# Performance work log

Hardware: AMD Instinct MI355X
Metric: run time of the kernel (lower is better)

## Reference

```python
import jax, jax.numpy as jnp
import numpy as np

EPS = 1e-12
HEADS = 16
DIM_KEYS = 16
DIM_VALUES = 64


def l2norm(t):
    # matches F.normalize(t, p=2, dim=-1) with eps=1e-12
    n = jnp.linalg.norm(t, axis=-1, keepdims=True)
    return t / jnp.maximum(n, EPS)


def tanh_norm(t):
    n = jnp.linalg.norm(t, axis=-1, keepdims=True)
    return jnp.tanh(n) * (t / jnp.maximum(n, EPS))


def split_heads(x, h):
    # [b, n, h*d] -> [b, h, n, d]
    b, n, hd = x.shape
    return x.reshape(b, n, h, hd // h).transpose(0, 2, 1, 3)


def setup_inputs() -> dict:
    key = jax.random.key(0)
    k1, k2, k3, k4 = jax.random.split(key, 4)
    b, n, dim = 4, 2048, 1024
    dim_inner = (DIM_KEYS + DIM_VALUES) * HEADS  # 1280
    tokens = jax.random.normal(k1, (b, n, dim), dtype=jnp.float32)
    Wqg = jax.random.normal(k2, (dim, dim_inner), dtype=jnp.float32) * (dim ** -0.5)
    Wkv = jax.random.normal(k3, (dim, dim_inner), dtype=jnp.float32) * (dim ** -0.5)
    Wout = jax.random.normal(k4, (DIM_VALUES * HEADS, dim), dtype=jnp.float32) * ((DIM_VALUES * HEADS) ** -0.5)
    return {"tokens": tokens, "Wqg": Wqg, "Wkv": Wkv, "Wout": Wout}


def reference(tokens, Wqg, Wkv, Wout):
    # self-attention variant: context = tokens, mask = None
    qg = split_heads(tokens @ Wqg, HEADS)   # [b, h, n, dk+dv]
    kv = split_heads(tokens @ Wkv, HEADS)
    queries, gates = qg[..., :DIM_KEYS], qg[..., DIM_KEYS:]
    keys, values = kv[..., :DIM_KEYS], kv[..., DIM_KEYS:]
    queries, keys, values = l2norm(queries), l2norm(keys), l2norm(values)
    sim = jnp.einsum('bhid,bhjd->bhij', queries, keys)
    attn = jnp.square(jax.nn.relu(sim))
    aggr = jnp.einsum('bhij,bhjd->bhid', attn, values)
    out = tanh_norm(aggr) * jnp.tanh(jax.nn.silu(gates))
    b, h, n, d = out.shape
    out = out.transpose(0, 2, 1, 3).reshape(b, n, h * d)  # merge heads
    return out @ Wout
```

## Files before the change

### kernel.cpp

```cpp
#include <hip/hip_runtime.h>
#include <cstdint>
#include <cstddef>

typedef __attribute__((ext_vector_type(8))) short short8;
typedef __attribute__((ext_vector_type(8))) unsigned short ushort8;
typedef __attribute__((ext_vector_type(4))) float f32x4;
typedef __attribute__((ext_vector_type(8))) _Float16 half8;
typedef __attribute__((ext_vector_type(2))) __fp16 fp16x2;

#define DEV static __device__ __forceinline__

DEV unsigned short f2bf(float x) {
  union { float f; unsigned u; } v; v.f = x;
  unsigned r = v.u + 0x7fffu + ((v.u >> 16) & 1u);
  return (unsigned short)(r >> 16);
}
DEV float bf2f(unsigned short u) {
  union { unsigned u; float f; } v; v.u = ((unsigned)u) << 16;
  return v.f;
}
DEV unsigned pack2bf(float lo, float hi) {
  union { float f; unsigned u; } a, b; a.f = lo; b.f = hi;
  return __builtin_amdgcn_perm(b.u + 0x8000u, a.u + 0x8000u, 0x07060302u);
}
DEV f32x4 mfma16(short8 a, short8 b, f32x4 c) {
  return __builtin_amdgcn_mfma_f32_16x16x32_bf16(a, b, c, 0, 0, 0);
}
DEV f32x4 mfma16h(half8 a, half8 b, f32x4 c) {
  return __builtin_amdgcn_mfma_f32_16x16x32_f16(a, b, c, 0, 0, 0);
}

typedef __attribute__((address_space(1))) unsigned int g_u32;
typedef __attribute__((address_space(3))) unsigned int l_u32;
DEV void glds16(const unsigned short* g, unsigned short* l) {
  __builtin_amdgcn_global_load_lds((g_u32*)g, (l_u32*)l, 16, 0, 0);
}

constexpr int Bc = 4, Nc = 2048, Dc = 1024, Hc = 16, DKc = 16, DVc = 64, DIc = 1280;
constexpr int Mc = Bc * Nc;

__global__ __launch_bounds__(256) void convert_x(const float* __restrict__ X,
                                                 unsigned short* __restrict__ Xb, int total8) {
  int i = blockIdx.x * 256 + threadIdx.x;
  if (i >= total8) return;
  const float4* p = (const float4*)(X + (size_t)i * 8);
  float4 a = p[0], b = p[1];
  ushort8 o;
  o[0] = f2bf(a.x); o[1] = f2bf(a.y); o[2] = f2bf(a.z); o[3] = f2bf(a.w);
  o[4] = f2bf(b.x); o[5] = f2bf(b.y); o[6] = f2bf(b.z); o[7] = f2bf(b.w);
  *(ushort8*)(Xb + (size_t)i * 8) = o;
}

__global__ __launch_bounds__(256) void transpose_convert(const float* __restrict__ W,
                                                         unsigned short* __restrict__ WT,
                                                         int K, int N) {
  __shared__ unsigned short t[64][72];
  int k0 = blockIdx.x * 64, n0 = blockIdx.y * 64;
  int tid = threadIdx.x;
#pragma unroll
  for (int it = 0; it < 16; ++it) {
    int f = it * 256 + tid;
    int r = f >> 6, c = f & 63;
    t[c][r] = f2bf(W[(size_t)(k0 + r) * N + n0 + c]);
  }
  __syncthreads();
#pragma unroll
  for (int it = 0; it < 16; ++it) {
    int f = it * 256 + tid;
    int r = f >> 6, c = f & 63;
    WT[(size_t)(n0 + r) * K + k0 + c] = t[r][c];
  }
}

__global__ __launch_bounds__(256) void gemm_proj(const unsigned short* __restrict__ A,
                                                 const unsigned short* __restrict__ BT,
                                                 unsigned short* __restrict__ QG,
                                                 unsigned short* __restrict__ KV,
                                                 int Kq) {
  __shared__ unsigned short As[128 * 64];
  __shared__ unsigned short Bs[128 * 64];
  int row0 = blockIdx.x * 128, col0 = blockIdx.y * 128;
  int tid = threadIdx.x, lane = tid & 63, wave = tid >> 6;
  int wm = wave >> 1, wn = wave & 1;
  int ql = lane >> 4, l16 = lane & 15;
  int r8 = lane >> 3, cbl = (lane & 7) ^ r8;

  unsigned short* dst = (col0 >= DIc) ? KV : QG;
  int c0l = (col0 >= DIc) ? col0 - DIc : col0;

  const unsigned short* gA = A + (size_t)(row0 + wave * 32 + r8) * Kq + cbl * 8;
  const unsigned short* gB = BT + (size_t)(col0 + wave * 32 + r8) * Kq + cbl * 8;

  f32x4 acc[4][4];
#pragma unroll
  for (int i = 0; i < 4; i++)
#pragma unroll
    for (int j = 0; j < 4; j++) acc[i][j] = (f32x4){0.f, 0.f, 0.f, 0.f};

  for (int k0 = 0; k0 < Kq; k0 += 64) {
    __syncthreads();
#pragma unroll
    for (int i = 0; i < 4; ++i) {
      glds16(gA + (size_t)(i * 8) * Kq + k0, &As[(wave * 32 + i * 8) * 64]);
      glds16(gB + (size_t)(i * 8) * Kq + k0, &Bs[(wave * 32 + i * 8) * 64]);
    }
    __syncthreads();
#pragma unroll
    for (int kk = 0; kk < 64; kk += 32) {
      short8 af[4], bfr[4];
#pragma unroll
      for (int t = 0; t < 4; t++) {
        int row = wm * 64 + t * 16 + l16;
        int cb = (kk >> 3) + ql;
        af[t] = *(const short8*)&As[row * 64 + ((cb ^ (row & 7)) << 3)];
      }
#pragma unroll
      for (int t = 0; t < 4; t++) {
        int row = wn * 64 + t * 16 + l16;
        int cb = (kk >> 3) + ql;
        bfr[t] = *(const short8*)&Bs[row * 64 + ((cb ^ (row & 7)) << 3)];
      }
#pragma unroll
      for (int i = 0; i < 4; i++)
#pragma unroll
        for (int j = 0; j < 4; j++) acc[i][j] = mfma16(af[i], bfr[j], acc[i][j]);
    }
  }
#pragma unroll
  for (int i = 0; i < 4; i++)
#pragma unroll
    for (int j = 0; j < 4; j++)
#pragma unroll
      for (int r = 0; r < 4; r++) {
        int rr = row0 + wm * 64 + i * 16 + ql * 4 + r;
        int cc = c0l + wn * 64 + j * 16 + l16;
        dst[(size_t)rr * DIc + cc] = f2bf(acc[i][j][r]);
      }
}

__global__ __launch_bounds__(256) void gemm_glds(const unsigned short* __restrict__ A,
                                                 const unsigned short* __restrict__ BT,
                                                 float* __restrict__ Cout,
                                                 int Mq, int Nq, int Kq) {
  __shared__ unsigned short As[128 * 64];
  __shared__ unsigned short Bs[128 * 64];
  int row0 = blockIdx.x * 128, col0 = blockIdx.y * 128;
  int tid = threadIdx.x, lane = tid & 63, wave = tid >> 6;
  int wm = wave >> 1, wn = wave & 1;
  int ql = lane >> 4, l16 = lane & 15;
  int r8 = lane >> 3, cbl = (lane & 7) ^ r8;

  const unsigned short* gA = A + (size_t)(row0 + wave * 32 + r8) * Kq + cbl * 8;
  const unsigned short* gB = BT + (size_t)(col0 + wave * 32 + r8) * Kq + cbl * 8;

  f32x4 acc[4][4];
#pragma unroll
  for (int i = 0; i < 4; i++)
#pragma unroll
    for (int j = 0; j < 4; j++) acc[i][j] = (f32x4){0.f, 0.f, 0.f, 0.f};

  for (int k0 = 0; k0 < Kq; k0 += 64) {
    __syncthreads();
#pragma unroll
    for (int i = 0; i < 4; ++i) {
      glds16(gA + (size_t)(i * 8) * Kq + k0, &As[(wave * 32 + i * 8) * 64]);
      glds16(gB + (size_t)(i * 8) * Kq + k0, &Bs[(wave * 32 + i * 8) * 64]);
    }
    __syncthreads();
#pragma unroll
    for (int kk = 0; kk < 64; kk += 32) {
      short8 af[4], bfr[4];
#pragma unroll
      for (int t = 0; t < 4; t++) {
        int row = wm * 64 + t * 16 + l16;
        int cb = (kk >> 3) + ql;
        af[t] = *(const short8*)&As[row * 64 + ((cb ^ (row & 7)) << 3)];
      }
#pragma unroll
      for (int t = 0; t < 4; t++) {
        int row = wn * 64 + t * 16 + l16;
        int cb = (kk >> 3) + ql;
        bfr[t] = *(const short8*)&Bs[row * 64 + ((cb ^ (row & 7)) << 3)];
      }
#pragma unroll
      for (int i = 0; i < 4; i++)
#pragma unroll
        for (int j = 0; j < 4; j++) acc[i][j] = mfma16(af[i], bfr[j], acc[i][j]);
    }
  }
#pragma unroll
  for (int i = 0; i < 4; i++)
#pragma unroll
    for (int j = 0; j < 4; j++)
#pragma unroll
      for (int r = 0; r < 4; r++) {
        int rr = row0 + wm * 64 + i * 16 + ql * 4 + r;
        int cc = col0 + wn * 64 + j * 16 + l16;
        Cout[(size_t)rr * Nq + cc] = acc[i][j][r];
      }
}

__global__ __launch_bounds__(256) void norm_kernel(const unsigned short* __restrict__ QG,
                                                   const unsigned short* __restrict__ KV,
                                                   unsigned short* __restrict__ Qn,
                                                   unsigned short* __restrict__ Kn,
                                                   unsigned short* __restrict__ Vtg)
{
  int g = blockIdx.x * 256 + threadIdx.x;
  int n = g & (Nc - 1), bh = g >> 11;
  int h = bh & 15, b = bh >> 4;
  size_t src = ((size_t)(b * Nc + n)) * DIc + h * 80;
  const ushort8 zeros = {0, 0, 0, 0, 0, 0, 0, 0};

  {
    ushort8 u0 = *(const ushort8*)&QG[src];
    ushort8 u1 = *(const ushort8*)&QG[src + 8];
    float q[16], ss = 0.f;
#pragma unroll
    for (int i = 0; i < 8; i++) { q[i] = bf2f(u0[i]); q[8 + i] = bf2f(u1[i]); }
#pragma unroll
    for (int i = 0; i < 16; i++) ss += q[i] * q[i];
    float sc = 1.f / fmaxf(sqrtf(ss), 1e-12f);
    half8 o0, o1;
#pragma unroll
    for (int i = 0; i < 8; i++) { o0[i] = (_Float16)(q[i] * sc); o1[i] = (_Float16)(q[8 + i] * sc); }
    size_t dst = ((size_t)bh * Nc + n) * 32;
    *(half8*)&Qn[dst] = o0;
    *(half8*)&Qn[dst + 8] = o1;
    *(ushort8*)&Qn[dst + 16] = zeros;
    *(ushort8*)&Qn[dst + 24] = zeros;
  }
  {
    ushort8 u0 = *(const ushort8*)&KV[src];
    ushort8 u1 = *(const ushort8*)&KV[src + 8];
    float q[16], ss = 0.f;
#pragma unroll
    for (int i = 0; i < 8; i++) { q[i] = bf2f(u0[i]); q[8 + i] = bf2f(u1[i]); }
#pragma unroll
    for (int i = 0; i < 16; i++) ss += q[i] * q[i];
    float sc = 1.f / fmaxf(sqrtf(ss), 1e-12f);
    half8 o0, o1;
#pragma unroll
    for (int i = 0; i < 8; i++) { o0[i] = (_Float16)(q[i] * sc); o1[i] = (_Float16)(q[8 + i] * sc); }
    size_t dst = ((size_t)bh * Nc + n) * 32;
    *(half8*)&Kn[dst] = o0;
    *(half8*)&Kn[dst + 8] = o1;
    *(ushort8*)&Kn[dst + 16] = zeros;
    *(ushort8*)&Kn[dst + 24] = zeros;
  }
  {
    ushort8 u[8];
#pragma unroll
    for (int i = 0; i < 8; i++) u[i] = *(const ushort8*)&KV[src + 16 + i * 8];
    float ss = 0.f;
#pragma unroll
    for (int i = 0; i < 8; i++)
#pragma unroll
      for (int j = 0; j < 8; j++) { float x = bf2f(u[i][j]); ss += x * x; }
    float sc = 1.f / fmaxf(sqrtf(ss), 1e-12f);
#pragma unroll
    for (int i = 0; i < 8; i++)
#pragma unroll
      for (int j = 0; j < 8; j++) {
        int d = i * 8 + j;
        union { _Float16 h; unsigned short us; } cv;
        cv.h = (_Float16)(bf2f(u[i][j]) * sc);
        Vtg[((size_t)bh * DVc + d) * Nc + n] = cv.us;
      }
  }
}

__global__ __launch_bounds__(256, 4) void attn_kernel(const unsigned short* __restrict__ Qn,
                                                      const unsigned short* __restrict__ Kn,
                                                      const unsigned short* __restrict__ Vtg,
                                                      const unsigned short* __restrict__ QG,
                                                      unsigned short* __restrict__ outpre) {
  __shared__ unsigned short shm[2 * 64 * 128];

  int gid = blockIdx.x;
  int xcd = gid & 7, slot = gid >> 3;
  int bh = xcd * 8 + (slot & 7);
  int q0 = (slot >> 3) * 128;
  int b = bh >> 4, h = bh & 15;
  int tid = threadIdx.x, lane = tid & 63, wave = tid >> 6;
  int ql = lane >> 4, l16 = lane & 15;
  int qw0 = q0 + wave * 32;

  half8 qf[2];
#pragma unroll
  for (int qt = 0; qt < 2; ++qt)
    qf[qt] = *(const half8*)&Qn[((size_t)bh * Nc + qw0 + qt * 16 + l16) * 32 + ql * 8];

  const unsigned short* krow = Kn + ((size_t)bh * Nc) * 32;
  const unsigned short* vbase = Vtg + ((size_t)bh * DVc) * Nc;

  int lr = lane >> 4, m16 = lane & 15;

  f32x4 acc[4][2];
#pragma unroll
  for (int dt = 0; dt < 4; dt++) { acc[dt][0] = (f32x4){0.f,0.f,0.f,0.f}; acc[dt][1] = (f32x4){0.f,0.f,0.f,0.f}; }

#pragma unroll
  for (int i = 0; i < 4; ++i) {
    int r0 = i * 16 + wave * 4;
    int d = r0 + lr;
    glds16(vbase + (size_t)d * Nc + 0 + ((m16 ^ (d & 7)) << 3), &shm[r0 * 128]);
  }

  for (int kt = 0; kt < Nc / 128; ++kt) {
    int k0 = kt * 128;
    unsigned short* vtb = &shm[(kt & 1) * 8192];
    __syncthreads();

    half8 kf[8];
#pragma unroll
    for (int kh = 0; kh < 8; ++kh)
      kf[kh] = *(const half8*)&krow[(size_t)(k0 + kh * 16 + l16) * 32 + ql * 8];

    if (kt < Nc / 128 - 1) {
      unsigned short* nb = &shm[((kt + 1) & 1) * 8192];
      int kn0 = k0 + 128;
#pragma unroll
      for (int i = 0; i < 4; ++i) {
        int r0 = i * 16 + wave * 4;
        int d = r0 + lr;
        glds16(vbase + (size_t)d * Nc + kn0 + ((m16 ^ (d & 7)) << 3), &nb[r0 * 128]);
      }
    }

#pragma unroll
    for (int p = 0; p < 4; ++p) {
      f32x4 c0[2], c1[2];
#pragma unroll
      for (int qt = 0; qt < 2; ++qt) {
        c0[qt] = mfma16h(kf[2 * p], qf[qt], (f32x4){0.f, 0.f, 0.f, 0.f});
        c1[qt] = mfma16h(kf[2 * p + 1], qf[qt], (f32x4){0.f, 0.f, 0.f, 0.f});
      }
      half8 pf[2];
#pragma unroll
      for (int qt = 0; qt < 2; ++qt) {
        union { half8 h; fp16x2 p2[4]; } w;
        fp16x2 t0 = __builtin_amdgcn_cvt_pkrtz(c0[qt][0], c0[qt][1]);
        fp16x2 t1 = __builtin_amdgcn_cvt_pkrtz(c0[qt][2], c0[qt][3]);
        fp16x2 t2 = __builtin_amdgcn_cvt_pkrtz(c1[qt][0], c1[qt][1]);
        fp16x2 t3 = __builtin_amdgcn_cvt_pkrtz(c1[qt][2], c1[qt][3]);
        const fp16x2 hz = {(__fp16)0, (__fp16)0};
        t0 = __builtin_elementwise_max(t0, hz); w.p2[0] = t0 * t0;
        t1 = __builtin_elementwise_max(t1, hz); w.p2[1] = t1 * t1;
        t2 = __builtin_elementwise_max(t2, hz); w.p2[2] = t2 * t2;
        t3 = __builtin_elementwise_max(t3, hz); w.p2[3] = t3 * t3;
        pf[qt] = w.h;
      }
      int tsw = (l16 & 7) << 1;
      int s1 = ((p * 8 + ql) ^ tsw) << 2;
      int s2 = ((p * 8 + 4 + ql) ^ tsw) << 2;
#pragma unroll
      for (int dt = 0; dt < 4; ++dt) {
        const unsigned short* vrow = vtb + (dt * 16 + l16) * 128;
        union { half8 s; uint4 u; } vf;
        uint2 va = *(const uint2*)&vrow[s1];
        uint2 vb2 = *(const uint2*)&vrow[s2];
        vf.u.x = va.x; vf.u.y = va.y; vf.u.z = vb2.x; vf.u.w = vb2.y;
#pragma unroll
        for (int qt = 0; qt < 2; ++qt) acc[dt][qt] = mfma16h(vf.s, pf[qt], acc[dt][qt]);
      }
    }
  }

  __syncthreads();
  unsigned short(*of)[68] = (unsigned short(*)[68])shm;

#pragma unroll
  for (int qt = 0; qt < 2; ++qt) {
    float ss = 0.f;
#pragma unroll
    for (int dt = 0; dt < 4; ++dt)
#pragma unroll
      for (int r = 0; r < 4; ++r) { float v = acc[dt][qt][r]; ss += v * v; }
    ss += __shfl_xor(ss, 16, 64);
    ss += __shfl_xor(ss, 32, 64);
    float nrm = sqrtf(ss);
    float sc = tanhf(nrm) / fmaxf(nrm, 1e-12f);
    int q = qw0 + qt * 16 + l16;
    size_t gbase = ((size_t)(b * Nc + q)) * DIc + h * 80 + DKc;
#pragma unroll
    for (int dt = 0; dt < 4; ++dt) {
      uint2 gu = *(const uint2*)&QG[gbase + dt * 16 + ql * 4];
      float o[4];
#pragma unroll
      for (int r = 0; r < 4; ++r) {
        unsigned short gb = (r < 2) ? (unsigned short)(gu.x >> (16 * r))
                                    : (unsigned short)(gu.y >> (16 * (r - 2)));
        float x = bf2f(gb);
        float s = x / (1.f + __expf(-x));
        float e2 = __expf(2.f * s);
        float g = 1.f - 2.f / (e2 + 1.f);
        o[r] = acc[dt][qt][r] * sc * g;
      }
      uint2 w;
      w.x = pack2bf(o[0], o[1]);
      w.y = pack2bf(o[2], o[3]);
      *(uint2*)&of[wave * 32 + qt * 16 + l16][dt * 16 + ql * 4] = w;
    }
  }
  __syncthreads();
  {
    int row = tid >> 1, cb = (tid & 1) * 32;
    size_t obase = ((size_t)(b * Nc + q0 + row)) * (Hc * DVc) + h * DVc + cb;
#pragma unroll
    for (int i = 0; i < 4; ++i)
      *(ushort8*)&outpre[obase + i * 8] = *(const ushort8*)&of[row][cb + i * 8];
  }
}

extern "C" void kernel_launch(void* const* d_in, const int* in_sizes, int n_in,
                              void* d_out, int out_size, void* d_ws, size_t ws_size,
                              hipStream_t stream) {
  const float* X = (const float*)d_in[0];
  const float* Wqg = (const float*)d_in[1];
  const float* Wkv = (const float*)d_in[2];
  const float* Wout = (const float*)d_in[3];
  float* out = (float*)d_out;
  (void)in_sizes; (void)n_in; (void)out_size; (void)ws_size;

  char* ws = (char*)d_ws;
  size_t off = 0;
  auto alloc = [&](size_t bytes) {
    void* p = ws + off;
    off += (bytes + 255) & ~(size_t)255;
    return p;
  };
  unsigned short* Xbf   = (unsigned short*)alloc((size_t)Mc * Dc * 2);
  unsigned short* WqgT  = (unsigned short*)alloc((size_t)DIc * Dc * 2);
  unsigned short* WkvT  = (unsigned short*)alloc((size_t)DIc * Dc * 2);
  unsigned short* WoutT = (unsigned short*)alloc((size_t)Dc * Dc * 2);
  unsigned short* QG    = (unsigned short*)alloc((size_t)Mc * DIc * 2);
  unsigned short* KV    = (unsigned short*)alloc((size_t)Mc * DIc * 2);
  unsigned short* Qn    = (unsigned short*)alloc((size_t)Bc * Hc * Nc * 32 * 2);
  unsigned short* Kn    = (unsigned short*)alloc((size_t)Bc * Hc * Nc * 32 * 2);
  unsigned short* Vtg   = (unsigned short*)alloc((size_t)Bc * Hc * Nc * DVc * 2);
  unsigned short* outpre = Xbf;

  convert_x<<<(Mc * Dc / 8) / 256, 256, 0, stream>>>(X, Xbf, Mc * Dc / 8);
  transpose_convert<<<dim3(Dc / 64, DIc / 64), 256, 0, stream>>>(Wqg, WqgT, Dc, DIc);
  transpose_convert<<<dim3(Dc / 64, DIc / 64), 256, 0, stream>>>(Wkv, WkvT, Dc, DIc);
  transpose_convert<<<dim3(Dc / 64, Dc / 64), 256, 0, stream>>>(Wout, WoutT, Dc, Dc);
  gemm_proj<<<dim3(Mc / 128, 2 * DIc / 128), 256, 0, stream>>>(Xbf, WqgT, QG, KV, Dc);
  norm_kernel<<<(Mc * Hc) / 256, 256, 0, stream>>>(QG, KV, Qn, Kn, Vtg);
  attn_kernel<<<1024, 256, 0, stream>>>(Qn, Kn, Vtg, QG, outpre);
  gemm_glds<<<dim3(Mc / 128, Dc / 128), 256, 0, stream>>>(outpre, WoutT, out, Mc, Dc, Dc);
}
```

Baseline: 262.3 us.

## Drop zero-padded Q/K, use 16x16x16 MFMA, register-staged V prefetch pipeline

Q and K are now stored as 16 fp16 values per row instead of being zero-padded to 32, which halves their memory footprint and the norm kernel's writes. The QK^T step uses the 16x16x16 f16 MFMA so no work is spent on the zero padding. V tiles are prefetched into registers and written to LDS with a new swizzle after compute, replacing the async global_load_lds path. The K-tile loop is unrolled by two with ping-pong K fragment registers, and s_setprio is raised around the PV MFMAs. The register staging raises register pressure, and the changed swizzle has to stay consistent between the LDS writes and reads.

```diff
diff --git a/kernel.cpp b/kernel.cpp
--- a/kernel.cpp
+++ b/kernel.cpp
@@ -6,6 +6,7 @@
 typedef __attribute__((ext_vector_type(8))) unsigned short ushort8;
 typedef __attribute__((ext_vector_type(4))) float f32x4;
 typedef __attribute__((ext_vector_type(8))) _Float16 half8;
+typedef __attribute__((ext_vector_type(4))) _Float16 half4;
 typedef __attribute__((ext_vector_type(2))) __fp16 fp16x2;
 
 #define DEV static __device__ __forceinline__
@@ -28,6 +29,9 @@
 }
 DEV f32x4 mfma16h(half8 a, half8 b, f32x4 c) {
   return __builtin_amdgcn_mfma_f32_16x16x32_f16(a, b, c, 0, 0, 0);
+}
+DEV f32x4 mfma16k(half4 a, half4 b, f32x4 c) {
+  return __builtin_amdgcn_mfma_f32_16x16x16f16(a, b, c, 0, 0, 0);
 }
 
 typedef __attribute__((address_space(1))) unsigned int g_u32;
@@ -210,7 +214,6 @@
   int n = g & (Nc - 1), bh = g >> 11;
   int h = bh & 15, b = bh >> 4;
   size_t src = ((size_t)(b * Nc + n)) * DIc + h * 80;
-  const ushort8 zeros = {0, 0, 0, 0, 0, 0, 0, 0};
 
   {
     ushort8 u0 = *(const ushort8*)&QG[src];
@@ -224,11 +227,9 @@
     half8 o0, o1;
 #pragma unroll
     for (int i = 0; i < 8; i++) { o0[i] = (_Float16)(q[i] * sc); o1[i] = (_Float16)(q[8 + i] * sc); }
-    size_t dst = ((size_t)bh * Nc + n) * 32;
+    size_t dst = ((size_t)bh * Nc + n) * 16;
     *(half8*)&Qn[dst] = o0;
     *(half8*)&Qn[dst + 8] = o1;
-    *(ushort8*)&Qn[dst + 16] = zeros;
-    *(ushort8*)&Qn[dst + 24] = zeros;
   }
   {
     ushort8 u0 = *(const ushort8*)&KV[src];
@@ -242,11 +243,9 @@
     half8 o0, o1;
 #pragma unroll
     for (int i = 0; i < 8; i++) { o0[i] = (_Float16)(q[i] * sc); o1[i] = (_Float16)(q[8 + i] * sc); }
-    size_t dst = ((size_t)bh * Nc + n) * 32;
+    size_t dst = ((size_t)bh * Nc + n) * 16;
     *(half8*)&Kn[dst] = o0;
     *(half8*)&Kn[dst + 8] = o1;
-    *(ushort8*)&Kn[dst + 16] = zeros;
-    *(ushort8*)&Kn[dst + 24] = zeros;
   }
   {
     ushort8 u[8];
@@ -286,86 +285,110 @@
   int ql = lane >> 4, l16 = lane & 15;
   int qw0 = q0 + wave * 32;
 
-  half8 qf[2];
+  half4 qf[2];
 #pragma unroll
   for (int qt = 0; qt < 2; ++qt)
-    qf[qt] = *(const half8*)&Qn[((size_t)bh * Nc + qw0 + qt * 16 + l16) * 32 + ql * 8];
-
-  const unsigned short* krow = Kn + ((size_t)bh * Nc) * 32;
+    qf[qt] = *(const half4*)&Qn[((size_t)bh * Nc + qw0 + qt * 16 + l16) * 16 + ql * 4];
+
+  const unsigned short* krow = Kn + (size_t)bh * Nc * 16;
   const unsigned short* vbase = Vtg + ((size_t)bh * DVc) * Nc;
 
-  int lr = lane >> 4, m16 = lane & 15;
+  int lq = lane >> 4, m16 = lane & 15;
+  unsigned swp = (unsigned)(lq & 1);
 
   f32x4 acc[4][2];
 #pragma unroll
   for (int dt = 0; dt < 4; dt++) { acc[dt][0] = (f32x4){0.f,0.f,0.f,0.f}; acc[dt][1] = (f32x4){0.f,0.f,0.f,0.f}; }
 
-#pragma unroll
-  for (int i = 0; i < 4; ++i) {
-    int r0 = i * 16 + wave * 4;
-    int d = r0 + lr;
-    glds16(vbase + (size_t)d * Nc + 0 + ((m16 ^ (d & 7)) << 3), &shm[r0 * 128]);
-  }
-
-  for (int kt = 0; kt < Nc / 128; ++kt) {
-    int k0 = kt * 128;
-    unsigned short* vtb = &shm[(kt & 1) * 8192];
-    __syncthreads();
-
-    half8 kf[8];
-#pragma unroll
-    for (int kh = 0; kh < 8; ++kh)
-      kf[kh] = *(const half8*)&krow[(size_t)(k0 + kh * 16 + l16) * 32 + ql * 8];
-
-    if (kt < Nc / 128 - 1) {
-      unsigned short* nb = &shm[((kt + 1) & 1) * 8192];
-      int kn0 = k0 + 128;
-#pragma unroll
-      for (int i = 0; i < 4; ++i) {
-        int r0 = i * 16 + wave * 4;
-        int d = r0 + lr;
-        glds16(vbase + (size_t)d * Nc + kn0 + ((m16 ^ (d & 7)) << 3), &nb[r0 * 128]);
-      }
-    }
-
-#pragma unroll
-    for (int p = 0; p < 4; ++p) {
-      f32x4 c0[2], c1[2];
-#pragma unroll
-      for (int qt = 0; qt < 2; ++qt) {
-        c0[qt] = mfma16h(kf[2 * p], qf[qt], (f32x4){0.f, 0.f, 0.f, 0.f});
-        c1[qt] = mfma16h(kf[2 * p + 1], qf[qt], (f32x4){0.f, 0.f, 0.f, 0.f});
-      }
-      half8 pf[2];
-#pragma unroll
-      for (int qt = 0; qt < 2; ++qt) {
-        union { half8 h; fp16x2 p2[4]; } w;
-        fp16x2 t0 = __builtin_amdgcn_cvt_pkrtz(c0[qt][0], c0[qt][1]);
-        fp16x2 t1 = __builtin_amdgcn_cvt_pkrtz(c0[qt][2], c0[qt][3]);
-        fp16x2 t2 = __builtin_amdgcn_cvt_pkrtz(c1[qt][0], c1[qt][1]);
-        fp16x2 t3 = __builtin_amdgcn_cvt_pkrtz(c1[qt][2], c1[qt][3]);
-        const fp16x2 hz = {(__fp16)0, (__fp16)0};
-        t0 = __builtin_elementwise_max(t0, hz); w.p2[0] = t0 * t0;
-        t1 = __builtin_elementwise_max(t1, hz); w.p2[1] = t1 * t1;
-        t2 = __builtin_elementwise_max(t2, hz); w.p2[2] = t2 * t2;
-        t3 = __builtin_elementwise_max(t3, hz); w.p2[3] = t3 * t3;
-        pf[qt] = w.h;
-      }
-      int tsw = (l16 & 7) << 1;
-      int s1 = ((p * 8 + ql) ^ tsw) << 2;
-      int s2 = ((p * 8 + 4 + ql) ^ tsw) << 2;
-#pragma unroll
-      for (int dt = 0; dt < 4; ++dt) {
-        const unsigned short* vrow = vtb + (dt * 16 + l16) * 128;
-        union { half8 s; uint4 u; } vf;
-        uint2 va = *(const uint2*)&vrow[s1];
-        uint2 vb2 = *(const uint2*)&vrow[s2];
-        vf.u.x = va.x; vf.u.y = va.y; vf.u.z = vb2.x; vf.u.w = vb2.y;
-#pragma unroll
-        for (int qt = 0; qt < 2; ++qt) acc[dt][qt] = mfma16h(vf.s, pf[qt], acc[dt][qt]);
-      }
-    }
-  }
+  half4 kfA[8], kfB[8];
+  uint4 vg[4];
+
+#pragma unroll
+  for (int kh = 0; kh < 8; ++kh)
+    kfA[kh] = *(const half4*)&krow[(size_t)(kh * 16 + l16) * 16 + ql * 4];
+#pragma unroll
+  for (int j = 0; j < 4; ++j) {
+    int r = wave * 16 + 4 * j + lq;
+    vg[j] = *(const uint4*)&vbase[(size_t)r * Nc + m16 * 8];
+  }
+#pragma unroll
+  for (int j = 0; j < 4; ++j) {
+    int r = wave * 16 + 4 * j + lq;
+    int M = m16 ^ ((r & 15) >> 1);
+    uint4 t = vg[j], o;
+    o.x = swp ? t.z : t.x; o.y = swp ? t.w : t.y;
+    o.z = swp ? t.x : t.z; o.w = swp ? t.y : t.w;
+    *(uint4*)&shm[r * 128 + M * 8] = o;
+  }
+
+#define TILE_BODY(KT, KFU, KFN, LN)                                                      \
+  {                                                                                      \
+    __syncthreads();                    \
+    unsigned short* vtb = &shm[((KT) & 1) * 8192];                                       \
+    unsigned short* vnb = &shm[(((KT) + 1) & 1) * 8192];                                 \
+    if (LN) {                                                                            \
+      int kn0 = ((KT) + 1) * 128;                                                        \
+      _Pragma("unroll") for (int kh = 0; kh < 8; ++kh)                                   \
+        KFN[kh] = *(const half4*)&krow[(size_t)(kn0 + kh * 16 + l16) * 16 + ql * 4];     \
+      _Pragma("unroll") for (int j = 0; j < 4; ++j) {                                    \
+        int r = wave * 16 + 4 * j + lq;                                                  \
+        vg[j] = *(const uint4*)&vbase[(size_t)r * Nc + kn0 + m16 * 8];                   \
+      }                                                                                  \
+    }                                                                                    \
+    _Pragma("unroll") for (int p = 0; p < 4; ++p) {                    \
+      f32x4 c0[2], c1[2];                                                                \
+      _Pragma("unroll") for (int qt = 0; qt < 2; ++qt) {                                 \
+        c0[qt] = mfma16k(KFU[2 * p],     qf[qt], (f32x4){0.f, 0.f, 0.f, 0.f});           \
+        c1[qt] = mfma16k(KFU[2 * p + 1], qf[qt], (f32x4){0.f, 0.f, 0.f, 0.f});           \
+      }                                                                                  \
+      half8 pf[2];                                                                       \
+      _Pragma("unroll") for (int qt = 0; qt < 2; ++qt) {                                 \
+        union { half8 hh; fp16x2 p2[4]; } w;                                             \
+        fp16x2 t0 = __builtin_amdgcn_cvt_pkrtz(c0[qt][0], c0[qt][1]);                    \
+        fp16x2 t1 = __builtin_amdgcn_cvt_pkrtz(c0[qt][2], c0[qt][3]);                    \
+        fp16x2 t2 = __builtin_amdgcn_cvt_pkrtz(c1[qt][0], c1[qt][1]);                    \
+        fp16x2 t3 = __builtin_amdgcn_cvt_pkrtz(c1[qt][2], c1[qt][3]);                    \
+        const fp16x2 hz = {(__fp16)0, (__fp16)0};                                        \
+        t0 = __builtin_elementwise_max(t0, hz); w.p2[0] = t0 * t0;                       \
+        t1 = __builtin_elementwise_max(t1, hz); w.p2[1] = t1 * t1;                       \
+        t2 = __builtin_elementwise_max(t2, hz); w.p2[2] = t2 * t2;                       \
+        t3 = __builtin_elementwise_max(t3, hz); w.p2[3] = t3 * t3;                       \
+        pf[qt] = w.hh;                                                                   \
+      }                                                                                  \
+                           \
+      int e1 = ((p * 8 + ql) ^ l16) << 2;                                                \
+      int e2 = e1 ^ 16;                                                                  \
+      __builtin_amdgcn_s_setprio(1);                                                     \
+      _Pragma("unroll") for (int dt = 0; dt < 4; ++dt) {                                 \
+        const unsigned short* vrow = vtb + (dt * 16 + l16) * 128;                        \
+        union { half8 s; uint4 u; } vf;                                                  \
+        uint2 va = *(const uint2*)&vrow[e1];                                             \
+        uint2 vb2 = *(const uint2*)&vrow[e2];                                            \
+        vf.u.x = va.x; vf.u.y = va.y; vf.u.z = vb2.x; vf.u.w = vb2.y;                    \
+        _Pragma("unroll") for (int qt = 0; qt < 2; ++qt)                                 \
+          acc[dt][qt] = mfma16h(vf.s, pf[qt], acc[dt][qt]);                              \
+      }                                                                                  \
+      __builtin_amdgcn_s_setprio(0);                                                     \
+    }                                                                                    \
+    if (LN) {             \
+      _Pragma("unroll") for (int j = 0; j < 4; ++j) {                                    \
+        int r = wave * 16 + 4 * j + lq;                                                  \
+        int M = m16 ^ ((r & 15) >> 1);                                                   \
+        uint4 t = vg[j], o;                                                              \
+        o.x = swp ? t.z : t.x; o.y = swp ? t.w : t.y;                                    \
+        o.z = swp ? t.x : t.z; o.w = swp ? t.y : t.w;                                    \
+        *(uint4*)&vnb[r * 128 + M * 8] = o;                                              \
+      }                                                                                  \
+    }                                                                                    \
+  }
+
+#pragma unroll 1
+  for (int kt2 = 0; kt2 < 8; ++kt2) {
+    int kte = kt2 * 2;
+    TILE_BODY(kte, kfA, kfB, 1)
+    TILE_BODY(kte + 1, kfB, kfA, (kt2 < 7))
+  }
+#undef TILE_BODY
 
   __syncthreads();
   unsigned short(*of)[68] = (unsigned short(*)[68])shm;
@@ -436,8 +459,8 @@
   unsigned short* WoutT = (unsigned short*)alloc((size_t)Dc * Dc * 2);
   unsigned short* QG    = (unsigned short*)alloc((size_t)Mc * DIc * 2);
   unsigned short* KV    = (unsigned short*)alloc((size_t)Mc * DIc * 2);
-  unsigned short* Qn    = (unsigned short*)alloc((size_t)Bc * Hc * Nc * 32 * 2);
-  unsigned short* Kn    = (unsigned short*)alloc((size_t)Bc * Hc * Nc * 32 * 2);
+  unsigned short* Qn    = (unsigned short*)alloc((size_t)Bc * Hc * Nc * 16 * 2);
+  unsigned short* Kn    = (unsigned short*)alloc((size_t)Bc * Hc * Nc * 16 * 2);
   unsigned short* Vtg   = (unsigned short*)alloc((size_t)Bc * Hc * Nc * DVc * 2);
   unsigned short* outpre = Xbf;
 
```

Result: no change. 261.4 us (-0.3%).
